# Kernel tuning notes

Hardware: AMD Instinct MI355X
Metric: run time of the kernel (lower is better)

## Reference

```python
import jax, jax.numpy as jnp
import numpy as np
from jax import lax

B, C_IN, C_MID, C_OUT, H, W = 8, 256, 128, 256, 128, 128
DN = ('NCHW', 'OIHW', 'NCHW')


def conv_bn(x, w, scale, shift, pad, relu):
    # conv (bias=False) + eval-mode BatchNorm folded to per-channel scale/shift
    y = lax.conv_general_dilated(x, w, (1, 1), [(pad, pad), (pad, pad)],
                                 dimension_numbers=DN)
    y = y * scale[None, :, None, None] + shift[None, :, None, None]
    return jax.nn.relu(y) if relu else y


def setup_inputs() -> dict:
    key = jax.random.key(0)
    ks = jax.random.split(key, 20)
    d = {"x": jax.random.normal(ks[0], (B, C_IN, H, W), dtype=jnp.float32)}
    f = 0.05  # weight scale
    def wparams(i, cout, cin, k):
        kk = jax.random.split(ks[i], 3)
        return (jax.random.normal(kk[0], (cout, cin, k, k), jnp.float32) * f,
                1.0 + 0.1 * jax.random.normal(kk[1], (cout,), jnp.float32),
                0.1 * jax.random.normal(kk[2], (cout,), jnp.float32))
    d["w_l"], d["s_l"], d["o_l"] = wparams(1, C_MID, C_IN, 3)
    d["w_r"], d["s_r"], d["o_r"] = wparams(2, C_MID, C_IN, 3)
    d["w_t"], d["s_t"], d["o_t"] = wparams(3, C_MID, C_IN, 3)
    d["w_b"], d["s_b"], d["o_b"] = wparams(4, C_MID, C_IN, 3)
    d["w2"], d["s2"], d["o2"] = wparams(5, C_OUT, C_MID, 3)
    d["w1"], d["s1"], d["o1"] = wparams(6, C_IN, C_IN, 1)
    return d


def reference(x, w_l, s_l, o_l, w_r, s_r, o_r, w_t, s_t, o_t,
              w_b, s_b, o_b, w2, s2, o2, w1, s1, o1):
    # four directional branches: conv+bn+relu then corner pooling (cummax scan)
    xl = lax.cummax(conv_bn(x, w_l, s_l, o_l, 1, True), axis=3, reverse=True)  # left: max over w'>=w
    xr = lax.cummax(conv_bn(x, w_r, s_r, o_r, 1, True), axis=3)                # right: max over w'<=w
    xt = lax.cummax(conv_bn(x, w_t, s_t, o_t, 1, True), axis=2, reverse=True)  # top: max over h'>=h
    xb = lax.cummax(conv_bn(x, w_b, s_b, o_b, 1, True), axis=2)                # bottom: max over h'<=h
    x1 = conv_bn(xl + xr + xb + xt, w2, s2, o2, 1, False)  # 3x3 conv+bn, no relu
    x2 = conv_bn(x, w1, s1, o1, 0, False)                  # 1x1 conv+bn skip, no relu
    return jax.nn.relu(x1 + x2)
```

## Files before the change

### kernel.cpp

```cpp
#include <hip/hip_runtime.h>

#define NEG_INF (-3.402823466e+38f)

typedef __bf16 bf16x8 __attribute__((ext_vector_type(8)));
typedef float  f32x16 __attribute__((ext_vector_type(16)));

__device__ __forceinline__ unsigned short f2bf(float f){
    unsigned u = __builtin_bit_cast(unsigned, f);
    u += 0x7fffu + ((u >> 16) & 1u);
    return (unsigned short)(u >> 16);
}
__device__ __forceinline__ float bf2f(unsigned short h){
    unsigned u = ((unsigned)h) << 16;
    return __builtin_bit_cast(float, u);
}

#if defined(__has_builtin)
#if __has_builtin(__builtin_amdgcn_global_load_lds)
#define ASYNC_CP 1
#endif
#endif

__device__ __forceinline__ void gl_lds(const unsigned short* g, unsigned short* lbase, int lane) {
#ifdef ASYNC_CP
    __builtin_amdgcn_global_load_lds(
        (const __attribute__((address_space(1))) unsigned int*)g,
        (__attribute__((address_space(3))) unsigned int*)lbase, 16, 0, 0);
#else
    *(uint4*)(lbase + (size_t)lane * 8) = *(const uint4*)g;
#endif
}

__global__ void __launch_bounds__(256)
k_xpose(const float* __restrict__ x, unsigned short* __restrict__ xh)
{
    __shared__ float tile[64 * 129];
    const int t = threadIdx.x;
    const int ci0 = blockIdx.x * 64, h = blockIdx.y, b = blockIdx.z;
    const float4* src = (const float4*)x;
#pragma unroll
    for (int i = 0; i < 8; ++i) {
        int idx = t + i * 256;
        int ci = idx >> 5, w4 = idx & 31;
        float4 v = src[((b * 256 + ci0 + ci) * 128 + h) * 32 + w4];
        tile[ci * 129 + w4 * 4 + 0] = v.x;
        tile[ci * 129 + w4 * 4 + 1] = v.y;
        tile[ci * 129 + w4 * 4 + 2] = v.z;
        tile[ci * 129 + w4 * 4 + 3] = v.w;
    }
    __syncthreads();
    unsigned* dst = (unsigned*)xh;
#pragma unroll
    for (int i = 0; i < 16; ++i) {
        int idx = t + i * 256;
        int w = idx >> 5, cp = idx & 31;
        float lo = tile[(cp * 2 + 0) * 129 + w];
        float hi = tile[(cp * 2 + 1) * 129 + w];
        dst[((b * 128 + h) * 128 + w) * 128 + (ci0 >> 1) + cp] =
            (unsigned)f2bf(lo) | ((unsigned)f2bf(hi) << 16);
    }
}

__global__ void __launch_bounds__(256)
k_wpack(const float* __restrict__ wl, const float* __restrict__ sl, const float* __restrict__ ol,
        const float* __restrict__ wr, const float* __restrict__ sr, const float* __restrict__ orr,
        const float* __restrict__ wt, const float* __restrict__ st, const float* __restrict__ ot,
        const float* __restrict__ wb, const float* __restrict__ sb, const float* __restrict__ ob,
        const float* __restrict__ w2, const float* __restrict__ s2, const float* __restrict__ o2,
        const float* __restrict__ w1, const float* __restrict__ s1, const float* __restrict__ o1,
        unsigned short* __restrict__ wpkBR, unsigned short* __restrict__ wpk2,
        unsigned short* __restrict__ wpk1, float* __restrict__ shF, float* __restrict__ obF)
{
    int i = blockIdx.x * 256 + threadIdx.x;
    if (i < 1179648) {
        int br = i / 294912, r = i % 294912;
        int c = r / 2304, r2 = r % 2304, ci = r2 / 9, k9 = r2 % 9;
        const float* wp = br == 0 ? wl : br == 1 ? wr : br == 2 ? wt : wb;
        const float* sp = br == 0 ? sl : br == 1 ? sr : br == 2 ? st : sb;
        float v = wp[r] * sp[c];
        int p = (c >> 4) * 64 + br * 16 + (c & 15);
        wpkBR[(((((ci >> 4) * 9 + k9) * 2 + ((ci >> 3) & 1)) * 512 + p) * 8) + (ci & 7)] = f2bf(v);
    } else if (i < 1474560) {
        int j = i - 1179648;
        int c = j / 1152, r2 = j % 1152, ci = r2 / 9, k9 = r2 % 9;
        wpk2[(((((ci >> 4) * 9 + k9) * 2 + ((ci >> 3) & 1)) * 256 + c) * 8) + (ci & 7)] = f2bf(w2[j] * s2[c]);
    } else if (i < 1540096) {
        int j = i - 1474560;
        int c = j >> 8, ci = j & 255;
        wpk1[((((ci >> 4) * 2 + ((ci >> 3) & 1)) * 256 + c) * 8) + (ci & 7)] = f2bf(w1[j] * s1[c]);
    } else if (i < 1540608) {
        int p = i - 1540096;
        int br = (p >> 4) & 3, c = (p >> 6) * 16 + (p & 15);
        const float* op = br == 0 ? ol : br == 1 ? orr : br == 2 ? ot : ob;
        shF[p] = op[c];
    } else if (i < 1540864) {
        int c = i - 1540608;
        obF[c] = o2[c] + o1[c];
    }
}

#define XIN_SH 12672
#define WBUF_SH 9216
__global__ void __launch_bounds__(256, 2)
k_brconv(const unsigned short* __restrict__ xh, const unsigned short* __restrict__ wpkBR,
         const float* __restrict__ shF, unsigned short* __restrict__ sbuf2,
         unsigned short* __restrict__ ytbT, unsigned short* __restrict__ ytbB)
{
    __shared__ __align__(16) unsigned short smem[2 * XIN_SH + WBUF_SH + 128];
    unsigned short* xinA = smem;
    unsigned short* xinB = smem + XIN_SH;
    unsigned short* wbuf = smem + 2 * XIN_SH;
    float* shs = (float*)(smem + 2 * XIN_SH + WBUF_SH);

    const int t = threadIdx.x;
    const int lin = (int)blockIdx.x + ((int)blockIdx.y << 3) + ((int)blockIdx.z << 8);
    const int swz = (lin & 7) * 256 + (lin >> 3);
    const int bx = swz & 7, h0 = ((swz >> 3) & 31) << 2, b = swz >> 8;
    const int wv = t >> 6, lane = t & 63;
    const int lo5 = lane & 31, hi1 = lane >> 5;
    const int hi32 = lane & 32;

    if (t < 64) shs[t] = shF[bx * 64 + t];
    for (int idx = t; idx < 3168; idx += 256)
        *(uint4*)(smem + idx * 8) = make_uint4(0, 0, 0, 0);

    f32x16 acc[2][4];
#pragma unroll
    for (int ct = 0; ct < 2; ++ct)
#pragma unroll
        for (int nb = 0; nb < 4; ++nb)
#pragma unroll
            for (int i = 0; i < 16; ++i) acc[ct][nb][i] = 0.f;

    __syncthreads();

    for (int s = wv; s < 24; s += 4) {
        int r = s >> 2, khi = (s >> 1) & 1, half = s & 1;
        int ih = h0 - 1 + r;
        if (ih >= 0 && ih < 128)
            gl_lds(xh + (((size_t)(b * 128 + ih) * 128 + half * 64 + lane) * 256) + khi * 8,
                   xinA + ((r * 2 + khi) * 132 + 1 + half * 64) * 8, lane);
    }
    for (int s = wv; s < 18; s += 4)
        gl_lds(wpkBR + ((size_t)s * 512 + bx * 64 + lane) * 8, wbuf + s * 512, lane);
    __syncthreads();

    uint4 wr0 = make_uint4(0, 0, 0, 0), wr1 = wr0, wr2 = wr0, wr3 = wr0, wr4 = wr0;
    unsigned short* xcur = xinA;
    unsigned short* xnxt = xinB;

    for (int cb = 0; cb < 16; ++cb) {
        if (cb < 15) {
            const int nc = cb + 1;
            for (int s = wv; s < 24; s += 4) {
                int r = s >> 2, khi = (s >> 1) & 1, half = s & 1;
                int ih = h0 - 1 + r;
                if (ih >= 0 && ih < 128)
                    gl_lds(xh + (((size_t)(b * 128 + ih) * 128 + half * 64 + lane) * 256) + nc * 16 + khi * 8,
                           xnxt + ((r * 2 + khi) * 132 + 1 + half * 64) * 8, lane);
            }
            wr0 = *(const uint4*)(wpkBR + ((size_t)(nc * 18 + wv) * 512 + bx * 64 + lane) * 8);
            wr1 = *(const uint4*)(wpkBR + ((size_t)(nc * 18 + wv + 4) * 512 + bx * 64 + lane) * 8);
            wr2 = *(const uint4*)(wpkBR + ((size_t)(nc * 18 + wv + 8) * 512 + bx * 64 + lane) * 8);
            wr3 = *(const uint4*)(wpkBR + ((size_t)(nc * 18 + wv + 12) * 512 + bx * 64 + lane) * 8);
            if (wv < 2)
                wr4 = *(const uint4*)(wpkBR + ((size_t)(nc * 18 + wv + 16) * 512 + bx * 64 + lane) * 8);
        }
#pragma unroll
        for (int k9 = 0; k9 < 9; ++k9) {
            const int kh = k9 / 3, kw = k9 % 3;
            bf16x8 a0 = *(const bf16x8*)(wbuf + ((k9 * 2 + hi1) * 64 + lo5) * 8);
            bf16x8 a1 = *(const bf16x8*)(wbuf + ((k9 * 2 + hi1) * 64 + 32 + lo5) * 8);
#pragma unroll
            for (int nb = 0; nb < 4; ++nb) {
                bf16x8 bf = *(const bf16x8*)(xcur + (((wv + kh) * 2 + hi1) * 132 + nb * 32 + lo5 + kw) * 8);
                acc[0][nb] = __builtin_amdgcn_mfma_f32_32x32x16_bf16(a0, bf, acc[0][nb], 0, 0, 0);
                acc[1][nb] = __builtin_amdgcn_mfma_f32_32x32x16_bf16(a1, bf, acc[1][nb], 0, 0, 0);
            }
        }
        __syncthreads();
        if (cb < 15) {
            *(uint4*)(wbuf + (wv) * 512 + lane * 8) = wr0;
            *(uint4*)(wbuf + (wv + 4) * 512 + lane * 8) = wr1;
            *(uint4*)(wbuf + (wv + 8) * 512 + lane * 8) = wr2;
            *(uint4*)(wbuf + (wv + 12) * 512 + lane * 8) = wr3;
            if (wv < 2)
                *(uint4*)(wbuf + (wv + 16) * 512 + lane * 8) = wr4;
            __syncthreads();
            unsigned short* tp = xcur; xcur = xnxt; xnxt = tp;
        }
    }

    unsigned short* pbw = smem + wv * 3072;
    const int hg = h0 + wv;

#pragma unroll
    for (int r = 0; r < 8; ++r) {
        const int m = (r & 3) + 8 * (r >> 2) + 4 * hi1;
        const float shv = shs[m];
        float carry = NEG_INF;
#pragma unroll
        for (int nn = 3; nn >= 0; --nn) {
            float a = fmaxf(acc[0][nn][r] + shv, 0.f);
#pragma unroll
            for (int d = 1; d < 32; d <<= 1) {
                float o = __shfl_down(a, d);
                if (lo5 < 32 - d) a = fmaxf(a, o);
            }
            a = fmaxf(a, carry);
            carry = __shfl(a, hi32);
            acc[0][nn][r] = a;
        }
    }
#pragma unroll
    for (int r = 8; r < 16; ++r) {
        const int m = 16 + (r & 3) + 8 * ((r >> 2) & 1) + 4 * hi1;
        const float shv = shs[m];
        float carry = NEG_INF;
#pragma unroll
        for (int nn = 0; nn < 4; ++nn) {
            float a = fmaxf(acc[0][nn][r] + shv, 0.f);
#pragma unroll
            for (int d = 1; d < 32; d <<= 1) {
                float o = __shfl_up(a, d);
                if (lo5 >= d) a = fmaxf(a, o);
            }
            a = fmaxf(a, carry);
            carry = __shfl(a, hi32 | 31);
            acc[0][nn][r] = a;
        }
    }
#pragma unroll
    for (int r = 0; r < 8; ++r) {
        const int c16 = (r & 3) + 8 * (r >> 2) + 4 * hi1;
#pragma unroll
        for (int nn = 0; nn < 4; ++nn)
            pbw[(nn * 32 + lo5) * 24 + c16] = f2bf(acc[0][nn][r] + acc[0][nn][r + 8]);
    }
    {
        unsigned short* gdst = sbuf2 + ((size_t)(b * 128 + hg) * 128) * 128 + bx * 16;
#pragma unroll
        for (int i = 0; i < 4; ++i) {
            int idx = lane + i * 64;
            int w = idx >> 1, part = idx & 1;
            *(uint4*)(gdst + (size_t)w * 128 + part * 8) = *(const uint4*)(pbw + w * 24 + part * 8);
        }
    }
#pragma unroll
    for (int r = 0; r < 8; ++r) {
        const int c16 = (r & 3) + 8 * (r >> 2) + 4 * hi1;
        const float shv = shs[32 + c16];
#pragma unroll
        for (int nn = 0; nn < 4; ++nn)
            pbw[(nn * 32 + lo5) * 24 + c16] = f2bf(fmaxf(acc[1][nn][r] + shv, 0.f));
    }
    {
        unsigned short* gdst = ytbT + ((size_t)(b * 128 + hg) * 128) * 128 + bx * 16;
#pragma unroll
        for (int i = 0; i < 4; ++i) {
            int idx = lane + i * 64;
            int w = idx >> 1, part = idx & 1;
            *(uint4*)(gdst + (size_t)w * 128 + part * 8) = *(const uint4*)(pbw + w * 24 + part * 8);
        }
    }
#pragma unroll
    for (int r = 8; r < 16; ++r) {
        const int c16 = (r & 3) + 8 * ((r >> 2) & 1) + 4 * hi1;
        const float shv = shs[48 + c16];
#pragma unroll
        for (int nn = 0; nn < 4; ++nn)
            pbw[(nn * 32 + lo5) * 24 + c16] = f2bf(fmaxf(acc[1][nn][r] + shv, 0.f));
    }
    {
        unsigned short* gdst = ytbB + ((size_t)(b * 128 + hg) * 128) * 128 + bx * 16;
#pragma unroll
        for (int i = 0; i < 4; ++i) {
            int idx = lane + i * 64;
            int w = idx >> 1, part = idx & 1;
            *(uint4*)(gdst + (size_t)w * 128 + part * 8) = *(const uint4*)(pbw + w * 24 + part * 8);
        }
    }
}

template<int REV>
__global__ void __launch_bounds__(256)
k_colscan(const unsigned short* __restrict__ ytb, unsigned short* __restrict__ sbuf2)
{
    __shared__ float tile[8][8][33];
    const int t = threadIdx.x;
    const int w0 = blockIdx.x * 8, c0 = blockIdx.y * 32, b = blockIdx.z;
    const int sc = t & 31, sw = t >> 5;
    const int rh = t >> 5, r5 = t & 31;
    const int rw = r5 >> 2, rcq = r5 & 3;
    float cum = NEG_INF;
    for (int step = 0; step < 16; ++step) {
        int h0 = REV ? 120 - step * 8 : step * 8;
        for (int q = 0; q < 8; ++q) {
            int hh = REV ? 7 - q : q;
            int hg = h0 + hh;
            float v = bf2f(ytb[((b * 128 + hg) * 128 + (w0 + sw)) * 128 + c0 + sc]);
            cum = fmaxf(cum, v);
            tile[hh][sw][sc] = cum;
        }
        __syncthreads();
        {
            int hg = h0 + rh;
            unsigned short* p = sbuf2 + ((b * 128 + hg) * 128 + w0 + rw) * 128 + c0 + rcq * 8;
            uint4 u = *(uint4*)p;
            unsigned short* us = (unsigned short*)&u;
#pragma unroll
            for (int j = 0; j < 8; ++j)
                us[j] = f2bf(bf2f(us[j]) + tile[rh][rw][rcq * 8 + j]);
            *(uint4*)p = u;
        }
        __syncthreads();
    }
}

__global__ void __launch_bounds__(256, 2)
k_final(const unsigned short* __restrict__ sbuf2, const unsigned short* __restrict__ xh,
        const unsigned short* __restrict__ wpk2, const unsigned short* __restrict__ wpk1,
        const float* __restrict__ obF, float* __restrict__ out)
{
    __shared__ __align__(16) unsigned short smem[2 * XIN_SH + WBUF_SH + 128];
    unsigned short* xinA = smem;
    unsigned short* xinB = smem + XIN_SH;
    unsigned short* wbuf = smem + 2 * XIN_SH;
    float* obs = (float*)(smem + 2 * XIN_SH + WBUF_SH);

    const int t = threadIdx.x;
    const int lin = (int)blockIdx.x + ((int)blockIdx.y << 2) + ((int)blockIdx.z << 7);
    const int swz = (lin & 7) * 128 + (lin >> 3);
    const int bx = swz & 3, h0 = ((swz >> 2) & 31) << 2, b = swz >> 7;
    const int wv = t >> 6, lane = t & 63;
    const int lo5 = lane & 31, hi1 = lane >> 5;

    if (t < 64) obs[t] = obF[bx * 64 + t];
    for (int idx = t; idx < 3168; idx += 256)
        *(uint4*)(smem + idx * 8) = make_uint4(0, 0, 0, 0);

    f32x16 acc[2][4];
#pragma unroll
    for (int ct = 0; ct < 2; ++ct)
#pragma unroll
        for (int nb = 0; nb < 4; ++nb)
#pragma unroll
            for (int i = 0; i < 16; ++i) acc[ct][nb][i] = 0.f;

    __syncthreads();

    for (int s = wv; s < 24; s += 4) {
        int r = s >> 2, khi = (s >> 1) & 1, half = s & 1;
        int ih = h0 - 1 + r;
        if (ih >= 0 && ih < 128)
            gl_lds(sbuf2 + (((size_t)(b * 128 + ih) * 128 + half * 64 + lane) * 128) + khi * 8,
                   xinA + ((r * 2 + khi) * 132 + 1 + half * 64) * 8, lane);
    }
    for (int s = wv; s < 18; s += 4)
        gl_lds(wpk2 + ((size_t)s * 256 + bx * 64 + lane) * 8, wbuf + s * 512, lane);
    __syncthreads();

    uint4 wr0 = make_uint4(0, 0, 0, 0), wr1 = wr0, wr2 = wr0, wr3 = wr0, wr4 = wr0;
    unsigned short* xcur = xinA;
    unsigned short* xnxt = xinB;

    for (int cb = 0; cb < 8; ++cb) {
        if (cb < 7) {
            const int nc = cb + 1;
            for (int s = wv; s < 24; s += 4) {
                int r = s >> 2, khi = (s >> 1) & 1, half = s & 1;
                int ih = h0 - 1 + r;
                if (ih >= 0 && ih < 128)
                    gl_lds(sbuf2 + (((size_t)(b * 128 + ih) * 128 + half * 64 + lane) * 128) + nc * 16 + khi * 8,
                           xnxt + ((r * 2 + khi) * 132 + 1 + half * 64) * 8, lane);
            }
            wr0 = *(const uint4*)(wpk2 + ((size_t)(nc * 18 + wv) * 256 + bx * 64 + lane) * 8);
            wr1 = *(const uint4*)(wpk2 + ((size_t)(nc * 18 + wv + 4) * 256 + bx * 64 + lane) * 8);
            wr2 = *(const uint4*)(wpk2 + ((size_t)(nc * 18 + wv + 8) * 256 + bx * 64 + lane) * 8);
            wr3 = *(const uint4*)(wpk2 + ((size_t)(nc * 18 + wv + 12) * 256 + bx * 64 + lane) * 8);
            if (wv < 2)
                wr4 = *(const uint4*)(wpk2 + ((size_t)(nc * 18 + wv + 16) * 256 + bx * 64 + lane) * 8);
        }
#pragma unroll
        for (int k9 = 0; k9 < 9; ++k9) {
            const int kh = k9 / 3, kw = k9 % 3;
            bf16x8 a0 = *(const bf16x8*)(wbuf + ((k9 * 2 + hi1) * 64 + lo5) * 8);
            bf16x8 a1 = *(const bf16x8*)(wbuf + ((k9 * 2 + hi1) * 64 + 32 + lo5) * 8);
#pragma unroll
            for (int nb = 0; nb < 4; ++nb) {
                bf16x8 bf = *(const bf16x8*)(xcur + (((wv + kh) * 2 + hi1) * 132 + nb * 32 + lo5 + kw) * 8);
                acc[0][nb] = __builtin_amdgcn_mfma_f32_32x32x16_bf16(a0, bf, acc[0][nb], 0, 0, 0);
                acc[1][nb] = __builtin_amdgcn_mfma_f32_32x32x16_bf16(a1, bf, acc[1][nb], 0, 0, 0);
            }
        }
        __syncthreads();
        if (cb < 7) {
            *(uint4*)(wbuf + (wv) * 512 + lane * 8) = wr0;
            *(uint4*)(wbuf + (wv + 4) * 512 + lane * 8) = wr1;
            *(uint4*)(wbuf + (wv + 8) * 512 + lane * 8) = wr2;
            *(uint4*)(wbuf + (wv + 12) * 512 + lane * 8) = wr3;
            if (wv < 2)
                *(uint4*)(wbuf + (wv + 16) * 512 + lane * 8) = wr4;
            __syncthreads();
            unsigned short* tp = xcur; xcur = xnxt; xnxt = tp;
        }
    }

    for (int s = wv; s < 16; s += 4) {
        int wr_ = s >> 2, khi = (s >> 1) & 1, half = s & 1;
        int ih = h0 + wr_;
        gl_lds(xh + (((size_t)(b * 128 + ih) * 128 + half * 64 + lane) * 256) + khi * 8,
               xnxt + ((wr_ * 2 + khi) * 132 + 1 + half * 64) * 8, lane);
    }
    for (int s = wv; s < 2; s += 4)
        gl_lds(wpk1 + ((size_t)s * 256 + bx * 64 + lane) * 8, wbuf + s * 512, lane);
    __syncthreads();
    { unsigned short* tp = xcur; xcur = xnxt; xnxt = tp; }

    for (int cb = 0; cb < 16; ++cb) {
        if (cb < 15) {
            const int nc = cb + 1;
            for (int s = wv; s < 16; s += 4) {
                int wr_ = s >> 2, khi = (s >> 1) & 1, half = s & 1;
                int ih = h0 + wr_;
                gl_lds(xh + (((size_t)(b * 128 + ih) * 128 + half * 64 + lane) * 256) + nc * 16 + khi * 8,
                       xnxt + ((wr_ * 2 + khi) * 132 + 1 + half * 64) * 8, lane);
            }
            if (wv < 2)
                wr0 = *(const uint4*)(wpk1 + ((size_t)(nc * 2 + wv) * 256 + bx * 64 + lane) * 8);
        }
        {
            bf16x8 a0 = *(const bf16x8*)(wbuf + (hi1 * 64 + lo5) * 8);
            bf16x8 a1 = *(const bf16x8*)(wbuf + (hi1 * 64 + 32 + lo5) * 8);
#pragma unroll
            for (int nb = 0; nb < 4; ++nb) {
                bf16x8 bf = *(const bf16x8*)(xcur + ((wv * 2 + hi1) * 132 + 1 + nb * 32 + lo5) * 8);
                acc[0][nb] = __builtin_amdgcn_mfma_f32_32x32x16_bf16(a0, bf, acc[0][nb], 0, 0, 0);
                acc[1][nb] = __builtin_amdgcn_mfma_f32_32x32x16_bf16(a1, bf, acc[1][nb], 0, 0, 0);
            }
        }
        __syncthreads();
        if (cb < 15) {
            if (wv < 2) *(uint4*)(wbuf + wv * 512 + lane * 8) = wr0;
            __syncthreads();
            unsigned short* tp = xcur; xcur = xnxt; xnxt = tp;
        }
    }

    const int hg = h0 + wv;
#pragma unroll
    for (int ct = 0; ct < 2; ++ct)
#pragma unroll
        for (int r = 0; r < 16; ++r) {
            const int m = ct * 32 + (r & 3) + 8 * (r >> 2) + 4 * hi1;
            const float bias = obs[m];
#pragma unroll
            for (int nb = 0; nb < 4; ++nb)
                out[((size_t)(b * 256 + bx * 64 + m) * 128 + hg) * 128 + nb * 32 + lo5] =
                    fmaxf(acc[ct][nb][r] + bias, 0.f);
        }
}

extern "C" void kernel_launch(void* const* d_in, const int* in_sizes, int n_in,
                              void* d_out, int out_size, void* d_ws, size_t ws_size,
                              hipStream_t stream)
{
    const float* x   = (const float*)d_in[0];
    const float* w_l = (const float*)d_in[1];
    const float* s_l = (const float*)d_in[2];
    const float* o_l = (const float*)d_in[3];
    const float* w_r = (const float*)d_in[4];
    const float* s_r = (const float*)d_in[5];
    const float* o_r = (const float*)d_in[6];
    const float* w_t = (const float*)d_in[7];
    const float* s_t = (const float*)d_in[8];
    const float* o_t = (const float*)d_in[9];
    const float* w_b = (const float*)d_in[10];
    const float* s_b = (const float*)d_in[11];
    const float* o_b = (const float*)d_in[12];
    const float* w2  = (const float*)d_in[13];
    const float* s2  = (const float*)d_in[14];
    const float* o2  = (const float*)d_in[15];
    const float* w1  = (const float*)d_in[16];
    const float* s1  = (const float*)d_in[17];
    const float* o1  = (const float*)d_in[18];
    float* out = (float*)d_out;
    char*  ws  = (char*)d_ws;

    unsigned short* xh    = (unsigned short*)(ws + 0);
    unsigned short* sbuf2 = (unsigned short*)(ws + 67108864);
    unsigned short* wpkBR = (unsigned short*)(ws + 100663296);
    unsigned short* wpk2  = (unsigned short*)(ws + 103022592);
    unsigned short* wpk1  = (unsigned short*)(ws + 103612416);
    float* shF = (float*)(ws + 103743488);
    float* obF = (float*)(ws + 103745536);

    unsigned short* ytbT = (unsigned short*)d_out;
    unsigned short* ytbB = ytbT + 16777216;

    dim3 blk(256);
    k_xpose<<<dim3(4, 128, 8), blk, 0, stream>>>(x, xh);
    k_wpack<<<dim3(6019), blk, 0, stream>>>(w_l, s_l, o_l, w_r, s_r, o_r,
                                            w_t, s_t, o_t, w_b, s_b, o_b,
                                            w2, s2, o2, w1, s1, o1,
                                            wpkBR, wpk2, wpk1, shF, obF);
    k_brconv<<<dim3(8, 32, 8), blk, 0, stream>>>(xh, wpkBR, shF, sbuf2, ytbT, ytbB);
    k_colscan<1><<<dim3(16, 4, 8), blk, 0, stream>>>(ytbT, sbuf2);
    k_colscan<0><<<dim3(16, 4, 8), blk, 0, stream>>>(ytbB, sbuf2);
    k_final<<<dim3(4, 32, 8), blk, 0, stream>>>(sbuf2, xh, wpk2, wpk1, obF, out);
}
```

Measured before the change: 692.0 us.

## Load conv weights directly into registers and drop LDS weight buffer

Both conv kernels now read each chunk's weight fragments from global memory straight into registers instead of staging them through an LDS buffer. This removes the LDS weight buffer, one barrier per chunk and the register-to-LDS copy. The smaller LDS footprint lets the launch bounds ask for 3 blocks per CU instead of 2. The 1x1 skip conv in the final kernel also reads x directly from global memory rather than through double-buffered LDS. In exchange, weight loads are no longer prefetched a chunk ahead, so their latency is exposed at the start of each chunk, and the 18 held fragments add register pressure.

```diff
diff --git a/kernel.cpp b/kernel.cpp
--- a/kernel.cpp
+++ b/kernel.cpp
@@ -100,17 +100,15 @@
 }
 
 #define XIN_SH 12672
-#define WBUF_SH 9216
-__global__ void __launch_bounds__(256, 2)
+__global__ void __launch_bounds__(256, 3)
 k_brconv(const unsigned short* __restrict__ xh, const unsigned short* __restrict__ wpkBR,
          const float* __restrict__ shF, unsigned short* __restrict__ sbuf2,
          unsigned short* __restrict__ ytbT, unsigned short* __restrict__ ytbB)
 {
-    __shared__ __align__(16) unsigned short smem[2 * XIN_SH + WBUF_SH + 128];
+    __shared__ __align__(16) unsigned short smem[2 * XIN_SH + 128];
     unsigned short* xinA = smem;
     unsigned short* xinB = smem + XIN_SH;
-    unsigned short* wbuf = smem + 2 * XIN_SH;
-    float* shs = (float*)(smem + 2 * XIN_SH + WBUF_SH);
+    float* shs = (float*)(smem + 2 * XIN_SH);
 
     const int t = threadIdx.x;
     const int lin = (int)blockIdx.x + ((int)blockIdx.y << 3) + ((int)blockIdx.z << 8);
@@ -141,15 +139,22 @@
             gl_lds(xh + (((size_t)(b * 128 + ih) * 128 + half * 64 + lane) * 256) + khi * 8,
                    xinA + ((r * 2 + khi) * 132 + 1 + half * 64) * 8, lane);
     }
-    for (int s = wv; s < 18; s += 4)
-        gl_lds(wpkBR + ((size_t)s * 512 + bx * 64 + lane) * 8, wbuf + s * 512, lane);
     __syncthreads();
 
-    uint4 wr0 = make_uint4(0, 0, 0, 0), wr1 = wr0, wr2 = wr0, wr3 = wr0, wr4 = wr0;
     unsigned short* xcur = xinA;
     unsigned short* xnxt = xinB;
 
     for (int cb = 0; cb < 16; ++cb) {
+        bf16x8 af0[9], af1[9];
+        {
+            const unsigned short* wp = wpkBR + ((size_t)(cb * 18 + hi1) * 512 + bx * 64) * 8;
+#pragma unroll
+            for (int k9 = 0; k9 < 9; ++k9) {
+                af0[k9] = *(const bf16x8*)(wp + lo5 * 8);
+                af1[k9] = *(const bf16x8*)(wp + (32 + lo5) * 8);
+                wp += 8192;
+            }
+        }
         if (cb < 15) {
             const int nc = cb + 1;
             for (int s = wv; s < 24; s += 4) {
@@ -159,36 +164,19 @@
                     gl_lds(xh + (((size_t)(b * 128 + ih) * 128 + half * 64 + lane) * 256) + nc * 16 + khi * 8,
                            xnxt + ((r * 2 + khi) * 132 + 1 + half * 64) * 8, lane);
             }
-            wr0 = *(const uint4*)(wpkBR + ((size_t)(nc * 18 + wv) * 512 + bx * 64 + lane) * 8);
-            wr1 = *(const uint4*)(wpkBR + ((size_t)(nc * 18 + wv + 4) * 512 + bx * 64 + lane) * 8);
-            wr2 = *(const uint4*)(wpkBR + ((size_t)(nc * 18 + wv + 8) * 512 + bx * 64 + lane) * 8);
-            wr3 = *(const uint4*)(wpkBR + ((size_t)(nc * 18 + wv + 12) * 512 + bx * 64 + lane) * 8);
-            if (wv < 2)
-                wr4 = *(const uint4*)(wpkBR + ((size_t)(nc * 18 + wv + 16) * 512 + bx * 64 + lane) * 8);
         }
 #pragma unroll
         for (int k9 = 0; k9 < 9; ++k9) {
             const int kh = k9 / 3, kw = k9 % 3;
-            bf16x8 a0 = *(const bf16x8*)(wbuf + ((k9 * 2 + hi1) * 64 + lo5) * 8);
-            bf16x8 a1 = *(const bf16x8*)(wbuf + ((k9 * 2 + hi1) * 64 + 32 + lo5) * 8);
 #pragma unroll
             for (int nb = 0; nb < 4; ++nb) {
                 bf16x8 bf = *(const bf16x8*)(xcur + (((wv + kh) * 2 + hi1) * 132 + nb * 32 + lo5 + kw) * 8);
-                acc[0][nb] = __builtin_amdgcn_mfma_f32_32x32x16_bf16(a0, bf, acc[0][nb], 0, 0, 0);
-                acc[1][nb] = __builtin_amdgcn_mfma_f32_32x32x16_bf16(a1, bf, acc[1][nb], 0, 0, 0);
+                acc[0][nb] = __builtin_amdgcn_mfma_f32_32x32x16_bf16(af0[k9], bf, acc[0][nb], 0, 0, 0);
+                acc[1][nb] = __builtin_amdgcn_mfma_f32_32x32x16_bf16(af1[k9], bf, acc[1][nb], 0, 0, 0);
             }
         }
         __syncthreads();
-        if (cb < 15) {
-            *(uint4*)(wbuf + (wv) * 512 + lane * 8) = wr0;
-            *(uint4*)(wbuf + (wv + 4) * 512 + lane * 8) = wr1;
-            *(uint4*)(wbuf + (wv + 8) * 512 + lane * 8) = wr2;
-            *(uint4*)(wbuf + (wv + 12) * 512 + lane * 8) = wr3;
-            if (wv < 2)
-                *(uint4*)(wbuf + (wv + 16) * 512 + lane * 8) = wr4;
-            __syncthreads();
-            unsigned short* tp = xcur; xcur = xnxt; xnxt = tp;
-        }
+        unsigned short* tp = xcur; xcur = xnxt; xnxt = tp;
     }
 
     unsigned short* pbw = smem + wv * 3072;
@@ -317,16 +305,15 @@
     }
 }
 
-__global__ void __launch_bounds__(256, 2)
+__global__ void __launch_bounds__(256, 3)
 k_final(const unsigned short* __restrict__ sbuf2, const unsigned short* __restrict__ xh,
         const unsigned short* __restrict__ wpk2, const unsigned short* __restrict__ wpk1,
         const float* __restrict__ obF, float* __restrict__ out)
 {
-    __shared__ __align__(16) unsigned short smem[2 * XIN_SH + WBUF_SH + 128];
+    __shared__ __align__(16) unsigned short smem[2 * XIN_SH + 128];
     unsigned short* xinA = smem;
     unsigned short* xinB = smem + XIN_SH;
-    unsigned short* wbuf = smem + 2 * XIN_SH;
-    float* obs = (float*)(smem + 2 * XIN_SH + WBUF_SH);
+    float* obs = (float*)(smem + 2 * XIN_SH);
 
     const int t = threadIdx.x;
     const int lin = (int)blockIdx.x + ((int)blockIdx.y << 2) + ((int)blockIdx.z << 7);
@@ -356,15 +343,22 @@
             gl_lds(sbuf2 + (((size_t)(b * 128 + ih) * 128 + half * 64 + lane) * 128) + khi * 8,
                    xinA + ((r * 2 + khi) * 132 + 1 + half * 64) * 8, lane);
     }
-    for (int s = wv; s < 18; s += 4)
-        gl_lds(wpk2 + ((size_t)s * 256 + bx * 64 + lane) * 8, wbuf + s * 512, lane);
     __syncthreads();
 
-    uint4 wr0 = make_uint4(0, 0, 0, 0), wr1 = wr0, wr2 = wr0, wr3 = wr0, wr4 = wr0;
     unsigned short* xcur = xinA;
     unsigned short* xnxt = xinB;
 
     for (int cb = 0; cb < 8; ++cb) {
+        bf16x8 af0[9], af1[9];
+        {
+            const unsigned short* wp = wpk2 + ((size_t)(cb * 18 + hi1) * 256 + bx * 64) * 8;
+#pragma unroll
+            for (int k9 = 0; k9 < 9; ++k9) {
+                af0[k9] = *(const bf16x8*)(wp + lo5 * 8);
+                af1[k9] = *(const bf16x8*)(wp + (32 + lo5) * 8);
+                wp += 4096;
+            }
+        }
         if (cb < 7) {
             const int nc = cb + 1;
             for (int s = wv; s < 24; s += 4) {
@@ -374,76 +368,34 @@
                     gl_lds(sbuf2 + (((size_t)(b * 128 + ih) * 128 + half * 64 + lane) * 128) + nc * 16 + khi * 8,
                            xnxt + ((r * 2 + khi) * 132 + 1 + half * 64) * 8, lane);
             }
-            wr0 = *(const uint4*)(wpk2 + ((size_t)(nc * 18 + wv) * 256 + bx * 64 + lane) * 8);
-            wr1 = *(const uint4*)(wpk2 + ((size_t)(nc * 18 + wv + 4) * 256 + bx * 64 + lane) * 8);
-            wr2 = *(const uint4*)(wpk2 + ((size_t)(nc * 18 + wv + 8) * 256 + bx * 64 + lane) * 8);
-            wr3 = *(const uint4*)(wpk2 + ((size_t)(nc * 18 + wv + 12) * 256 + bx * 64 + lane) * 8);
-            if (wv < 2)
-                wr4 = *(const uint4*)(wpk2 + ((size_t)(nc * 18 + wv + 16) * 256 + bx * 64 + lane) * 8);
         }
 #pragma unroll
         for (int k9 = 0; k9 < 9; ++k9) {
             const int kh = k9 / 3, kw = k9 % 3;
-            bf16x8 a0 = *(const bf16x8*)(wbuf + ((k9 * 2 + hi1) * 64 + lo5) * 8);
-            bf16x8 a1 = *(const bf16x8*)(wbuf + ((k9 * 2 + hi1) * 64 + 32 + lo5) * 8);
 #pragma unroll
             for (int nb = 0; nb < 4; ++nb) {
                 bf16x8 bf = *(const bf16x8*)(xcur + (((wv + kh) * 2 + hi1) * 132 + nb * 32 + lo5 + kw) * 8);
+                acc[0][nb] = __builtin_amdgcn_mfma_f32_32x32x16_bf16(af0[k9], bf, acc[0][nb], 0, 0, 0);
+                acc[1][nb] = __builtin_amdgcn_mfma_f32_32x32x16_bf16(af1[k9], bf, acc[1][nb], 0, 0, 0);
+            }
+        }
+        __syncthreads();
+        unsigned short* tp = xcur; xcur = xnxt; xnxt = tp;
+    }
+
+    {
+        const unsigned short* xrow = xh + ((size_t)(b * 128 + h0 + wv) * 128) * 256 + hi1 * 8;
+        const unsigned short* w1p  = wpk1 + ((size_t)hi1 * 256 + bx * 64) * 8;
+#pragma unroll 4
+        for (int cb = 0; cb < 16; ++cb) {
+            bf16x8 a0 = *(const bf16x8*)(w1p + ((size_t)cb * 512 + lo5) * 8);
+            bf16x8 a1 = *(const bf16x8*)(w1p + ((size_t)cb * 512 + 32 + lo5) * 8);
+#pragma unroll
+            for (int nb = 0; nb < 4; ++nb) {
+                bf16x8 bf = *(const bf16x8*)(xrow + (size_t)(nb * 32 + lo5) * 256 + cb * 16);
                 acc[0][nb] = __builtin_amdgcn_mfma_f32_32x32x16_bf16(a0, bf, acc[0][nb], 0, 0, 0);
                 acc[1][nb] = __builtin_amdgcn_mfma_f32_32x32x16_bf16(a1, bf, acc[1][nb], 0, 0, 0);
             }
-        }
-        __syncthreads();
-        if (cb < 7) {
-            *(uint4*)(wbuf + (wv) * 512 + lane * 8) = wr0;
-            *(uint4*)(wbuf + (wv + 4) * 512 + lane * 8) = wr1;
-            *(uint4*)(wbuf + (wv + 8) * 512 + lane * 8) = wr2;
-            *(uint4*)(wbuf + (wv + 12) * 512 + lane * 8) = wr3;
-            if (wv < 2)
-                *(uint4*)(wbuf + (wv + 16) * 512 + lane * 8) = wr4;
-            __syncthreads();
-            unsigned short* tp = xcur; xcur = xnxt; xnxt = tp;
-        }
-    }
-
-    for (int s = wv; s < 16; s += 4) {
-        int wr_ = s >> 2, khi = (s >> 1) & 1, half = s & 1;
-        int ih = h0 + wr_;
-        gl_lds(xh + (((size_t)(b * 128 + ih) * 128 + half * 64 + lane) * 256) + khi * 8,
-               xnxt + ((wr_ * 2 + khi) * 132 + 1 + half * 64) * 8, lane);
-    }
-    for (int s = wv; s < 2; s += 4)
-        gl_lds(wpk1 + ((size_t)s * 256 + bx * 64 + lane) * 8, wbuf + s * 512, lane);
-    __syncthreads();
-    { unsigned short* tp = xcur; xcur = xnxt; xnxt = tp; }
-
-    for (int cb = 0; cb < 16; ++cb) {
-        if (cb < 15) {
-            const int nc = cb + 1;
-            for (int s = wv; s < 16; s += 4) {
-                int wr_ = s >> 2, khi = (s >> 1) & 1, half = s & 1;
-                int ih = h0 + wr_;
-                gl_lds(xh + (((size_t)(b * 128 + ih) * 128 + half * 64 + lane) * 256) + nc * 16 + khi * 8,
-                       xnxt + ((wr_ * 2 + khi) * 132 + 1 + half * 64) * 8, lane);
-            }
-            if (wv < 2)
-                wr0 = *(const uint4*)(wpk1 + ((size_t)(nc * 2 + wv) * 256 + bx * 64 + lane) * 8);
-        }
-        {
-            bf16x8 a0 = *(const bf16x8*)(wbuf + (hi1 * 64 + lo5) * 8);
-            bf16x8 a1 = *(const bf16x8*)(wbuf + (hi1 * 64 + 32 + lo5) * 8);
-#pragma unroll
-            for (int nb = 0; nb < 4; ++nb) {
-                bf16x8 bf = *(const bf16x8*)(xcur + ((wv * 2 + hi1) * 132 + 1 + nb * 32 + lo5) * 8);
-                acc[0][nb] = __builtin_amdgcn_mfma_f32_32x32x16_bf16(a0, bf, acc[0][nb], 0, 0, 0);
-                acc[1][nb] = __builtin_amdgcn_mfma_f32_32x32x16_bf16(a1, bf, acc[1][nb], 0, 0, 0);
-            }
-        }
-        __syncthreads();
-        if (cb < 15) {
-            if (wv < 2) *(uint4*)(wbuf + wv * 512 + lane * 8) = wr0;
-            __syncthreads();
-            unsigned short* tp = xcur; xcur = xnxt; xnxt = tp;
         }
     }
 
```

After: 1.623 ms. 2.35x slower.
